# Optimization experiments

Measured on AMD Instinct MI355X. Metric: run time of the kernel, lower is better.

Reference implementation:

```python
import jax, jax.numpy as jnp
import numpy as np

H = 25   # num heads
D = 128  # head dim
EPS = 1e-6

def rmsnorm(x, w):
    # RMSNorm over last dim (hidden=3200), computed in fp32
    var = jnp.mean(jnp.square(x.astype(jnp.float32)), axis=-1, keepdims=True)
    return (x.astype(jnp.float32) * jax.lax.rsqrt(var + EPS)).astype(x.dtype) * w


def setup_inputs() -> dict:
    key = jax.random.key(0)
    ks = jax.random.split(key, 4)
    B, N, C = 8, 1025, 3200
    x = jax.random.normal(ks[0], (B, N, C), dtype=jnp.float32)
    w_qkv = jax.random.normal(ks[1], (3 * C, C), dtype=jnp.float32) * (C ** -0.5)
    q_norm_w = jnp.ones((C,), dtype=jnp.float32)
    k_norm_w = jnp.ones((C,), dtype=jnp.float32)
    w_proj = jax.random.normal(ks[2], (C, C), dtype=jnp.float32) * (C ** -0.5)
    b_proj = jnp.zeros((C,), dtype=jnp.float32)
    return {"x": x, "w_qkv": w_qkv, "q_norm_w": q_norm_w,
            "k_norm_w": k_norm_w, "w_proj": w_proj, "b_proj": b_proj}


def reference(x, w_qkv, q_norm_w, k_norm_w, w_proj, b_proj):
    B, N, C = x.shape
    # fused QKV projection: [B,N,3C]
    qkv = jnp.einsum('bnc,oc->bno', x, w_qkv)
    q, k, v = qkv[..., :C], qkv[..., C:2 * C], qkv[..., 2 * C:]
    # per-tensor RMSNorm over the full hidden dim (flattened across heads)
    q = rmsnorm(q, q_norm_w)
    k = rmsnorm(k, k_norm_w)
    # split heads: [B,N,H,D]
    q = q.reshape(B, N, H, D)
    k = k.reshape(B, N, H, D)
    v = v.reshape(B, N, H, D)
    scale = 1.0 / np.sqrt(D)
    scores = jnp.einsum('bqhd,bkhd->bhqk', q, k) * scale
    attn = jax.nn.softmax(scores, axis=-1)
    out = jnp.einsum('bhqk,bkhd->bqhd', attn, v).reshape(B, N, C)
    return jnp.einsum('bnc,oc->bno', out, w_proj) + b_proj
```

## Files before the change

kernel.cpp:

```cpp
#include <hip/hip_runtime.h>
#include <hip/hip_bf16.h>

#define B_     8
#define N_     1025
#define C_     3200
#define H_     25
#define D_     128
#define NQKV   (3 * C_)
#define NQKVP  9728
#define M_REAL (B_ * N_)
#define M_PAD  8448
#define KVB    64
#define KPAD   1088
#define CPADW  3328

typedef __bf16 bf16x8 __attribute__((ext_vector_type(8)));
typedef short  short8 __attribute__((ext_vector_type(8)));
typedef float  f32x4  __attribute__((ext_vector_type(4)));
typedef unsigned int u32x4 __attribute__((ext_vector_type(4)));

__device__ __forceinline__ unsigned short f2bf(float f) {
    unsigned u = __builtin_bit_cast(unsigned, f);
    u += 0x7FFFu + ((u >> 16) & 1u);
    return (unsigned short)(u >> 16);
}
__device__ __forceinline__ float bf2f(unsigned short u) {
    unsigned v = ((unsigned)u) << 16;
    return __builtin_bit_cast(float, v);
}
__device__ __forceinline__ unsigned cvtpk_bf16(float lo, float hi) {
    unsigned r;
    asm("v_cvt_pk_bf16_f32 %0, %1, %2" : "=v"(r) : "v"(lo), "v"(hi));
    return r;
}
__device__ __forceinline__ void gload_lds16(const unsigned short* g, void* lds) {
    __builtin_amdgcn_global_load_lds(
        (const __attribute__((address_space(1))) void*)g,
        (__attribute__((address_space(3))) void*)lds, 16, 0, 0);
}

__global__ __launch_bounds__(256) void convert_pad(const float* __restrict__ src,
                                                   unsigned short* __restrict__ dst,
                                                   long n_src, long n_tot) {
    long e = ((long)blockIdx.x * 256 + threadIdx.x) * 4;
    if (e >= n_tot) return;
    ushort4 o;
    if (e < n_src) {
        float4 v = *reinterpret_cast<const float4*>(src + e);
        o.x = f2bf(v.x); o.y = f2bf(v.y); o.z = f2bf(v.z); o.w = f2bf(v.w);
    } else {
        o.x = o.y = o.z = o.w = 0;
    }
    *reinterpret_cast<ushort4*>(dst + e) = o;
}

__global__ __launch_bounds__(256) void rmsnorm_qk(unsigned short* __restrict__ qkv,
                                                  const float* __restrict__ qw,
                                                  const float* __restrict__ kw) {
    const int row = blockIdx.x;
    const int seg = blockIdx.y;
    unsigned short* p = qkv + (long)row * NQKVP + seg * C_;
    const float* w = seg ? kw : qw;
    const int t = threadIdx.x;
    const bool has2 = t < (400 - 256);

    short8 v0 = reinterpret_cast<const short8*>(p)[t];
    short8 v1;
    if (has2) v1 = reinterpret_cast<const short8*>(p)[t + 256];

    float s = 0.f;
#pragma unroll
    for (int j = 0; j < 8; ++j) { float f = bf2f((unsigned short)v0[j]); s += f * f; }
    if (has2) {
#pragma unroll
        for (int j = 0; j < 8; ++j) { float f = bf2f((unsigned short)v1[j]); s += f * f; }
    }
#pragma unroll
    for (int m = 32; m; m >>= 1) s += __shfl_xor(s, m);
    __shared__ float red[4];
    if ((t & 63) == 0) red[t >> 6] = s;
    __syncthreads();
    float tot = red[0] + red[1] + red[2] + red[3];
    float scale = rsqrtf(tot * (1.f / C_) + 1e-6f);
    if (seg == 0) scale *= 0.08838834764831845f;

#pragma unroll
    for (int j = 0; j < 8; ++j) {
        float f = bf2f((unsigned short)v0[j]) * scale * w[t * 8 + j];
        v0[j] = (short)f2bf(f);
    }
    reinterpret_cast<short8*>(p)[t] = v0;
    if (has2) {
#pragma unroll
        for (int j = 0; j < 8; ++j) {
            float f = bf2f((unsigned short)v1[j]) * scale * w[(t + 256) * 8 + j];
            v1[j] = (short)f2bf(f);
        }
        reinterpret_cast<short8*>(p)[t + 256] = v1;
    }
}

#define BKT 32
template <int FP32OUT>
__global__ __launch_bounds__(512) void gemm_pipe(const unsigned short* __restrict__ A,
                                                 const unsigned short* __restrict__ Bm,
                                                 unsigned short* __restrict__ Cb,
                                                 float* __restrict__ Cf,
                                                 const float* __restrict__ bias,
                                                 int K, int MT, int NT, int ldc,
                                                 int MStore, int NStore) {
    __shared__ unsigned short sA[4][256 * BKT];
    __shared__ unsigned short sB[4][256 * BKT];

    int bid = blockIdx.x;
    int xcd = bid & 7, pos = bid >> 3;
    int nstrips = NT >> 3;
    int fullpos = nstrips * MT;
    int mt, nt;
    if (pos < fullpos) {
        int strip = pos / MT;
        mt = pos - strip * MT;
        nt = strip * 8 + xcd;
    } else {
        int lin = bid - fullpos * 8;
        nt = nstrips * 8 + lin / MT;
        mt = lin - (lin / MT) * MT;
    }
    const int m0 = mt * 256, n0 = nt * 256;

    const int t = threadIdx.x, w = t >> 6, l = t & 63;
    const int lq = l & 15, lh = l >> 4;
    const int wr = w >> 2, wc = w & 3;

    const unsigned short* Ab = A + (long)m0 * K;
    const unsigned short* Bb = Bm + (long)n0 * K;
    const int nk = K / BKT;

    const int c0 = t, c1 = t + 512;
    const int r0 = c0 >> 2, s0 = (c0 & 3) ^ ((r0 >> 1) & 3);
    const int r1 = c1 >> 2, s1 = (c1 & 3) ^ ((r1 >> 1) & 3);

    f32x4 acc[8][4] = {};

    auto stage = [&](int tile) {
        int k0 = tile * BKT;
        unsigned short* dA = sA[tile & 3];
        unsigned short* dB = sB[tile & 3];
        gload_lds16(Ab + (long)r0 * K + k0 + s0 * 8, (char*)dA + c0 * 16);
        gload_lds16(Ab + (long)r1 * K + k0 + s1 * 8, (char*)dA + c1 * 16);
        gload_lds16(Bb + (long)r0 * K + k0 + s0 * 8, (char*)dB + c0 * 16);
        gload_lds16(Bb + (long)r1 * K + k0 + s1 * 8, (char*)dB + c1 * 16);
    };

    stage(0); stage(1); stage(2);

    for (int tt = 0; tt < nk; ++tt) {
        if (tt + 2 < nk)      asm volatile("s_waitcnt vmcnt(8) lgkmcnt(0)" ::: "memory");
        else if (tt + 1 < nk) asm volatile("s_waitcnt vmcnt(4) lgkmcnt(0)" ::: "memory");
        else                  asm volatile("s_waitcnt vmcnt(0) lgkmcnt(0)" ::: "memory");
        __builtin_amdgcn_s_barrier();

        const unsigned short* bufA = sA[tt & 3];
        const unsigned short* bufB = sB[tt & 3];
        bf16x8 av[8], bv[4];
#pragma unroll
        for (int i = 0; i < 8; ++i) {
            int row = wr * 128 + i * 16 + lq;
            av[i] = *reinterpret_cast<const bf16x8*>(bufA + row * BKT + ((lh ^ ((row >> 1) & 3)) << 3));
        }
#pragma unroll
        for (int j = 0; j < 4; ++j) {
            int row = wc * 64 + j * 16 + lq;
            bv[j] = *reinterpret_cast<const bf16x8*>(bufB + row * BKT + ((lh ^ ((row >> 1) & 3)) << 3));
        }
        if (tt + 3 < nk) stage(tt + 3);

        __builtin_amdgcn_s_setprio(1);
#pragma unroll
        for (int i = 0; i < 8; ++i)
#pragma unroll
            for (int j = 0; j < 4; ++j)
                acc[i][j] = __builtin_amdgcn_mfma_f32_16x16x32_bf16(av[i], bv[j], acc[i][j], 0, 0, 0);
        __builtin_amdgcn_s_setprio(0);
    }

#pragma unroll
    for (int i = 0; i < 8; ++i) {
#pragma unroll
        for (int r2 = 0; r2 < 4; ++r2) {
            long grow = m0 + wr * 128 + i * 16 + lh * 4 + r2;
            if (FP32OUT && grow >= MStore) continue;
#pragma unroll
            for (int j = 0; j < 4; ++j) {
                int gcol = n0 + wc * 64 + j * 16 + lq;
                if (FP32OUT) {
                    if (gcol < NStore)
                        Cf[grow * ldc + gcol] = acc[i][j][r2] + bias[gcol];
                } else {
                    Cb[grow * ldc + gcol] = f2bf(acc[i][j][r2]);
                }
            }
        }
    }
}

__global__ __launch_bounds__(256) void v_transpose(const unsigned short* __restrict__ qkv,
                                                   unsigned short* __restrict__ vtb) {
    const int kt = blockIdx.x, h = blockIdx.y, b = blockIdx.z;
    const int t = threadIdx.x;
    __shared__ unsigned short tile[64][136];

    {
        int r = t >> 2, dq = (t & 3) * 32;
        int key = kt * 64 + r;
        int keyc = key < N_ ? key : N_ - 1;
        const unsigned short* src = qkv + ((long)(b * N_) + keyc) * NQKVP + 2 * C_ + h * D_ + dq;
        short8 a0 = *reinterpret_cast<const short8*>(src);
        short8 a1 = *reinterpret_cast<const short8*>(src + 8);
        short8 a2 = *reinterpret_cast<const short8*>(src + 16);
        short8 a3 = *reinterpret_cast<const short8*>(src + 24);
        if (key >= N_) { a0 = 0; a1 = 0; a2 = 0; a3 = 0; }
        *reinterpret_cast<short8*>(&tile[r][dq])      = a0;
        *reinterpret_cast<short8*>(&tile[r][dq + 8])  = a1;
        *reinterpret_cast<short8*>(&tile[r][dq + 16]) = a2;
        *reinterpret_cast<short8*>(&tile[r][dq + 24]) = a3;
    }
    __syncthreads();
    {
        int d = t >> 1, k0 = (t & 1) * 32;
        unsigned short* dst = vtb + ((long)(b * H_ + h) * D_ + d) * KPAD + kt * 64 + k0;
#pragma unroll
        for (int jj = 0; jj < 4; ++jj) {
            short8 g;
#pragma unroll
            for (int e = 0; e < 8; ++e) g[e] = (short)tile[k0 + jj * 8 + e][d];
            *reinterpret_cast<short8*>(dst + jj * 8) = g;
        }
    }
}

__global__ __launch_bounds__(256, 2) void attn_fwd(const unsigned short* __restrict__ qkv,
                                                   const unsigned short* __restrict__ vtb,
                                                   unsigned short* __restrict__ outb) {
    const int qt = blockIdx.x, h = blockIdx.y, b = blockIdx.z;
    const int t = threadIdx.x, w = t >> 6, l = t & 63;
    const int lq = l & 15, lh = l >> 4;

    __shared__ unsigned short sK[2][KVB * D_];
    __shared__ unsigned short sV[2][D_ * KVB];

    const int qbase = qt * 128 + w * 32;
    bf16x8 qf[2][4];
#pragma unroll
    for (int qg = 0; qg < 2; ++qg) {
        int qrow = qbase + qg * 16 + lq; if (qrow > N_ - 1) qrow = N_ - 1;
        const unsigned short* qp = qkv + (long)(b * N_ + qrow) * NQKVP + h * D_;
#pragma unroll
        for (int ds = 0; ds < 4; ++ds)
            qf[qg][ds] = *reinterpret_cast<const bf16x8*>(qp + ds * 32 + lh * 8);
    }

    const unsigned short* kp[4];
    const unsigned short* vp[4];
#pragma unroll
    for (int i = 0; i < 4; ++i) {
        int slot = i * 256 + t;
        { int r = slot >> 4, sd = (slot & 15) ^ (r & 7);
          kp[i] = qkv + ((long)(b * N_) + r) * NQKVP + C_ + h * D_ + sd * 8; }
        { int d = slot >> 3, sk = (slot & 7) ^ (d & 7);
          vp[i] = vtb + ((long)(b * H_ + h) * D_ + d) * KPAD + sk * 8; }
    }
    const long kvstep = 64L * NQKVP;

    auto stageK = [&](int tile, int buf) {
        char* dst = (char*)sK[buf];
        if (tile < 16) {
            long off = (long)tile * kvstep;
#pragma unroll
            for (int i = 0; i < 4; ++i) gload_lds16(kp[i] + off, dst + (i * 256 + t) * 16);
        } else {
#pragma unroll
            for (int i = 0; i < 4; ++i) {
                int slot = i * 256 + t;
                int r = slot >> 4, sd = (slot & 15) ^ (r & 7);
                const unsigned short* p = qkv + ((long)(b * N_) + (N_ - 1)) * NQKVP + C_ + h * D_ + sd * 8;
                gload_lds16(p, dst + slot * 16);
            }
        }
    };
    auto stageV = [&](int tile, int buf) {
        char* dst = (char*)sV[buf];
        long off = (long)tile * 64;
#pragma unroll
        for (int i = 0; i < 4; ++i) gload_lds16(vp[i] + off, dst + (i * 256 + t) * 16);
    };

    f32x4 o[2][8] = {};
    float m[2] = {-1e30f, -1e30f}, lsum[2] = {0.f, 0.f};

    stageK(0, 0); stageV(0, 0);

    for (int tt = 0; tt < 17; ++tt) {
        const int cur = tt & 1;
        if (tt < 16) { stageK(tt + 1, cur ^ 1); stageV(tt + 1, cur ^ 1); }
        if (tt < 16) asm volatile("s_waitcnt vmcnt(8)" ::: "memory");
        else         asm volatile("s_waitcnt vmcnt(0)" ::: "memory");
        __builtin_amdgcn_s_barrier();

        const unsigned short* bK = sK[cur];
        const unsigned short* bV = sV[cur];

        f32x4 s[2][4] = {};
#pragma unroll
        for (int c = 0; c < 4; ++c) {
            bf16x8 kf[4];
#pragma unroll
            for (int ds = 0; ds < 4; ++ds)
                kf[ds] = *reinterpret_cast<const bf16x8*>(
                    bK + (c * 16 + lq) * D_ + (((ds << 2) + lh) ^ (lq & 7)) * 8);
            __builtin_amdgcn_s_setprio(1);
#pragma unroll
            for (int qg = 0; qg < 2; ++qg)
#pragma unroll
                for (int ds = 0; ds < 4; ++ds)
                    s[qg][c] = __builtin_amdgcn_mfma_f32_16x16x32_bf16(kf[ds], qf[qg][ds], s[qg][c], 0, 0, 0);
            __builtin_amdgcn_s_setprio(0);
        }
        if (tt == 16) {
#pragma unroll
            for (int c = 0; c < 4; ++c)
#pragma unroll
                for (int r = 0; r < 4; ++r)
                    if (c * 16 + 4 * lh + r != 0) { s[0][c][r] = -1e30f; s[1][c][r] = -1e30f; }
        }

        bf16x8 pa[2][2];
#pragma unroll
        for (int qg = 0; qg < 2; ++qg) {
            float mx = s[qg][0][0];
#pragma unroll
            for (int c = 0; c < 4; ++c)
#pragma unroll
                for (int r = 0; r < 4; ++r) mx = fmaxf(mx, s[qg][c][r]);
            mx = fmaxf(mx, __shfl_xor(mx, 16));
            mx = fmaxf(mx, __shfl_xor(mx, 32));
            if (__any(mx - m[qg] > 8.0f)) {
                float mnew = fmaxf(m[qg], mx);
                float corr = __expf(m[qg] - mnew);
                lsum[qg] *= corr;
#pragma unroll
                for (int r = 0; r < 4; ++r) {
                    float co = __shfl(corr, lh * 4 + r);
#pragma unroll
                    for (int nf = 0; nf < 8; ++nf) o[qg][nf][r] *= co;
                }
                m[qg] = mnew;
            }
            float p[4][4]; float rs = 0.f;
#pragma unroll
            for (int c = 0; c < 4; ++c)
#pragma unroll
                for (int r = 0; r < 4; ++r) {
                    p[c][r] = __expf(s[qg][c][r] - m[qg]);
                    rs += p[c][r];
                }
            rs += __shfl_xor(rs, 16);
            rs += __shfl_xor(rs, 32);
            lsum[qg] += rs;
#pragma unroll
            for (int h2 = 0; h2 < 2; ++h2) {
                unsigned A0 = cvtpk_bf16(p[2 * h2][0], p[2 * h2][1]);
                unsigned A1 = cvtpk_bf16(p[2 * h2][2], p[2 * h2][3]);
                unsigned B0 = cvtpk_bf16(p[2 * h2 + 1][0], p[2 * h2 + 1][1]);
                unsigned B1 = cvtpk_bf16(p[2 * h2 + 1][2], p[2 * h2 + 1][3]);
                const bool lo2 = lh < 2, odd = lh & 1;
                unsigned x16_0 = __shfl_xor(lo2 ? A0 : B0, 16);
                unsigned x16_1 = __shfl_xor(lo2 ? A1 : B1, 16);
                unsigned x32_0 = __shfl_xor(lo2 ? B0 : A0, 32);
                unsigned x32_1 = __shfl_xor(lo2 ? B1 : A1, 32);
                unsigned x48_0 = __shfl_xor(odd ? B0 : A0, 48);
                unsigned x48_1 = __shfl_xor(odd ? B1 : A1, 48);
                unsigned w0 = lh == 0 ? A0 : lh == 1 ? x48_0 : lh == 2 ? x32_0 : x16_0;
                unsigned w1 = lh == 0 ? A1 : lh == 1 ? x48_1 : lh == 2 ? x32_1 : x16_1;
                unsigned w2 = lh == 0 ? x16_0 : lh == 1 ? x32_0 : lh == 2 ? x48_0 : B0;
                unsigned w3 = lh == 0 ? x16_1 : lh == 1 ? x32_1 : lh == 2 ? x48_1 : B1;
                u32x4 wv = {w0, w1, w2, w3};
                pa[qg][h2] = __builtin_bit_cast(bf16x8, wv);
            }
        }

#pragma unroll
        for (int h2 = 0; h2 < 2; ++h2) {
            bf16x8 vf[8];
#pragma unroll
            for (int nf = 0; nf < 8; ++nf)
                vf[nf] = *reinterpret_cast<const bf16x8*>(
                    bV + (nf * 16 + lq) * KVB + (((h2 << 2) + lh) ^ (lq & 7)) * 8);
            __builtin_amdgcn_s_setprio(1);
#pragma unroll
            for (int qg = 0; qg < 2; ++qg)
#pragma unroll
                for (int nf = 0; nf < 8; ++nf)
                    o[qg][nf] = __builtin_amdgcn_mfma_f32_16x16x32_bf16(pa[qg][h2], vf[nf], o[qg][nf], 0, 0, 0);
            __builtin_amdgcn_s_setprio(0);
        }
        __builtin_amdgcn_s_barrier();
    }

#pragma unroll
    for (int qg = 0; qg < 2; ++qg) {
        float linv = 1.f / lsum[qg];
#pragma unroll
        for (int r = 0; r < 4; ++r) {
            float li = __shfl(linv, lh * 4 + r);
            int row = qbase + qg * 16 + 4 * lh + r;
            if (row < N_) {
                unsigned short* dst = outb + (long)(b * N_ + row) * C_ + h * D_ + lq;
#pragma unroll
                for (int nf = 0; nf < 8; ++nf)
                    dst[nf * 16] = f2bf(o[qg][nf][r] * li);
            }
        }
    }
}

extern "C" void kernel_launch(void* const* d_in, const int* in_sizes, int n_in,
                              void* d_out, int out_size, void* d_ws, size_t ws_size,
                              hipStream_t stream) {
    (void)in_sizes; (void)n_in; (void)out_size; (void)ws_size;
    const float* x   = (const float*)d_in[0];
    const float* wq  = (const float*)d_in[1];
    const float* qnw = (const float*)d_in[2];
    const float* knw = (const float*)d_in[3];
    const float* wp  = (const float*)d_in[4];
    const float* bp  = (const float*)d_in[5];
    float* out = (float*)d_out;

    unsigned short* xb    = (unsigned short*)d_ws;
    unsigned short* wqb   = xb   + (size_t)M_PAD * C_;
    unsigned short* wpb   = wqb  + (size_t)NQKVP * C_;
    unsigned short* qkvb  = wpb  + (size_t)CPADW * C_;
    unsigned short* attnb = qkvb + (size_t)M_PAD * NQKVP;
    unsigned short* vtb   = wqb;

    auto cvt = [&](const float* s, unsigned short* d, long nsrc, long ntot) {
        int blocks = (int)((ntot / 4 + 255) / 256);
        convert_pad<<<blocks, 256, 0, stream>>>(s, d, nsrc, ntot);
    };
    cvt(x,  xb,  (long)M_REAL * C_, (long)M_PAD * C_);
    cvt(wq, wqb, (long)NQKV * C_,   (long)NQKVP * C_);
    cvt(wp, wpb, (long)C_ * C_,     (long)CPADW * C_);
    cvt(x, attnb + (size_t)M_REAL * C_, 0, (long)(M_PAD - M_REAL) * C_);

    gemm_pipe<0><<<(M_PAD / 256) * (NQKVP / 256), 512, 0, stream>>>(
        xb, wqb, qkvb, nullptr, nullptr, C_, M_PAD / 256, NQKVP / 256, NQKVP, M_PAD, NQKVP);

    rmsnorm_qk<<<dim3(M_REAL, 2), 256, 0, stream>>>(qkvb, qnw, knw);

    v_transpose<<<dim3(17, H_, B_), 256, 0, stream>>>(qkvb, vtb);

    attn_fwd<<<dim3(9, H_, B_), 256, 0, stream>>>(qkvb, vtb, attnb);

    gemm_pipe<1><<<(M_PAD / 256) * (CPADW / 256), 512, 0, stream>>>(
        attnb, wpb, nullptr, out, bp, C_, M_PAD / 256, CPADW / 256, C_, M_REAL, C_);
}
```

Baseline: 1.056 ms.

## Restructure GEMM main loop to BK=64 double buffer with four-phase compute interleaving

Moves the bf16 GEMM from a 4-stage BK=32 LDS ring to a 2-stage BK=64 double buffer, using 8-way XOR swizzled tiles. Each K iteration is split into four quadrant phases, each with its own LDS fragment reads, barriers and MFMA bursts, similar to a ping-pong schedule. The aim is fewer LDS fragment registers, fewer loop iterations per K, and overlap of LDS reads with MFMA work. The cost is a shallower global prefetch depth and many more barriers per iteration, which can expose memory latency.

```diff
diff --git a/kernel.cpp b/kernel.cpp
--- a/kernel.cpp
+++ b/kernel.cpp
@@ -100,7 +100,7 @@
     }
 }
 
-#define BKT 32
+#define BKT 64
 template <int FP32OUT>
 __global__ __launch_bounds__(512) void gemm_pipe(const unsigned short* __restrict__ A,
                                                  const unsigned short* __restrict__ Bm,
@@ -109,8 +109,8 @@
                                                  const float* __restrict__ bias,
                                                  int K, int MT, int NT, int ldc,
                                                  int MStore, int NStore) {
-    __shared__ unsigned short sA[4][256 * BKT];
-    __shared__ unsigned short sB[4][256 * BKT];
+    __shared__ unsigned short sA[2][256 * BKT];
+    __shared__ unsigned short sB[2][256 * BKT];
 
     int bid = blockIdx.x;
     int xcd = bid & 7, pos = bid >> 3;
@@ -136,53 +136,110 @@
     const unsigned short* Bb = Bm + (long)n0 * K;
     const int nk = K / BKT;
 
-    const int c0 = t, c1 = t + 512;
-    const int r0 = c0 >> 2, s0 = (c0 & 3) ^ ((r0 >> 1) & 3);
-    const int r1 = c1 >> 2, s1 = (c1 & 3) ^ ((r1 >> 1) & 3);
-
     f32x4 acc[8][4] = {};
 
     auto stage = [&](int tile) {
         int k0 = tile * BKT;
-        unsigned short* dA = sA[tile & 3];
-        unsigned short* dB = sB[tile & 3];
-        gload_lds16(Ab + (long)r0 * K + k0 + s0 * 8, (char*)dA + c0 * 16);
-        gload_lds16(Ab + (long)r1 * K + k0 + s1 * 8, (char*)dA + c1 * 16);
-        gload_lds16(Bb + (long)r0 * K + k0 + s0 * 8, (char*)dB + c0 * 16);
-        gload_lds16(Bb + (long)r1 * K + k0 + s1 * 8, (char*)dB + c1 * 16);
+        unsigned short* dA = sA[tile & 1];
+        unsigned short* dB = sB[tile & 1];
+#pragma unroll
+        for (int i = 0; i < 4; ++i) {
+            int c = i * 512 + t;
+            int row = c >> 3, sl = (c & 7) ^ (row & 7);
+            gload_lds16(Ab + (long)row * K + k0 + sl * 8, (char*)dA + c * 16);
+            gload_lds16(Bb + (long)row * K + k0 + sl * 8, (char*)dB + c * 16);
+        }
     };
 
-    stage(0); stage(1); stage(2);
+#define RD(buf, row, kk) \
+    (*reinterpret_cast<const bf16x8*>((buf) + (row) * BKT + (((((kk) << 2) + lh)) ^ ((row) & 7)) * 8))
+
+    stage(0);
+    asm volatile("s_waitcnt vmcnt(0)" ::: "memory");
+    __builtin_amdgcn_s_barrier();
 
     for (int tt = 0; tt < nk; ++tt) {
-        if (tt + 2 < nk)      asm volatile("s_waitcnt vmcnt(8) lgkmcnt(0)" ::: "memory");
-        else if (tt + 1 < nk) asm volatile("s_waitcnt vmcnt(4) lgkmcnt(0)" ::: "memory");
-        else                  asm volatile("s_waitcnt vmcnt(0) lgkmcnt(0)" ::: "memory");
-        __builtin_amdgcn_s_barrier();
-
-        const unsigned short* bufA = sA[tt & 3];
-        const unsigned short* bufB = sB[tt & 3];
-        bf16x8 av[8], bv[4];
-#pragma unroll
-        for (int i = 0; i < 8; ++i) {
+        const unsigned short* bufA = sA[tt & 1];
+        const unsigned short* bufB = sB[tt & 1];
+        bf16x8 av[4][2], bv[4][2];
+
+#pragma unroll
+        for (int i = 0; i < 4; ++i) {
             int row = wr * 128 + i * 16 + lq;
-            av[i] = *reinterpret_cast<const bf16x8*>(bufA + row * BKT + ((lh ^ ((row >> 1) & 3)) << 3));
-        }
-#pragma unroll
-        for (int j = 0; j < 4; ++j) {
+            av[i][0] = RD(bufA, row, 0); av[i][1] = RD(bufA, row, 1);
+        }
+#pragma unroll
+        for (int j = 0; j < 2; ++j) {
             int row = wc * 64 + j * 16 + lq;
-            bv[j] = *reinterpret_cast<const bf16x8*>(bufB + row * BKT + ((lh ^ ((row >> 1) & 3)) << 3));
-        }
-        if (tt + 3 < nk) stage(tt + 3);
-
+            bv[j][0] = RD(bufB, row, 0); bv[j][1] = RD(bufB, row, 1);
+        }
+        if (tt + 1 < nk) stage(tt + 1);
+        __builtin_amdgcn_s_barrier();
+        asm volatile("s_waitcnt lgkmcnt(0)" ::: "memory");
+        __builtin_amdgcn_sched_barrier(0);
         __builtin_amdgcn_s_setprio(1);
 #pragma unroll
-        for (int i = 0; i < 8; ++i)
-#pragma unroll
-            for (int j = 0; j < 4; ++j)
-                acc[i][j] = __builtin_amdgcn_mfma_f32_16x16x32_bf16(av[i], bv[j], acc[i][j], 0, 0, 0);
+        for (int i = 0; i < 4; ++i)
+#pragma unroll
+            for (int j = 0; j < 2; ++j) {
+                acc[i][j] = __builtin_amdgcn_mfma_f32_16x16x32_bf16(av[i][0], bv[j][0], acc[i][j], 0, 0, 0);
+                acc[i][j] = __builtin_amdgcn_mfma_f32_16x16x32_bf16(av[i][1], bv[j][1], acc[i][j], 0, 0, 0);
+            }
         __builtin_amdgcn_s_setprio(0);
-    }
+        __builtin_amdgcn_s_barrier();
+
+#pragma unroll
+        for (int j = 2; j < 4; ++j) {
+            int row = wc * 64 + j * 16 + lq;
+            bv[j][0] = RD(bufB, row, 0); bv[j][1] = RD(bufB, row, 1);
+        }
+        __builtin_amdgcn_s_barrier();
+        asm volatile("s_waitcnt lgkmcnt(0)" ::: "memory");
+        __builtin_amdgcn_sched_barrier(0);
+        __builtin_amdgcn_s_setprio(1);
+#pragma unroll
+        for (int i = 0; i < 4; ++i)
+#pragma unroll
+            for (int j = 2; j < 4; ++j) {
+                acc[i][j] = __builtin_amdgcn_mfma_f32_16x16x32_bf16(av[i][0], bv[j][0], acc[i][j], 0, 0, 0);
+                acc[i][j] = __builtin_amdgcn_mfma_f32_16x16x32_bf16(av[i][1], bv[j][1], acc[i][j], 0, 0, 0);
+            }
+        __builtin_amdgcn_s_setprio(0);
+        __builtin_amdgcn_s_barrier();
+
+#pragma unroll
+        for (int i = 0; i < 4; ++i) {
+            int row = wr * 128 + (i + 4) * 16 + lq;
+            av[i][0] = RD(bufA, row, 0); av[i][1] = RD(bufA, row, 1);
+        }
+        __builtin_amdgcn_s_barrier();
+        asm volatile("s_waitcnt lgkmcnt(0)" ::: "memory");
+        __builtin_amdgcn_sched_barrier(0);
+        __builtin_amdgcn_s_setprio(1);
+#pragma unroll
+        for (int i = 0; i < 4; ++i)
+#pragma unroll
+            for (int j = 2; j < 4; ++j) {
+                acc[i + 4][j] = __builtin_amdgcn_mfma_f32_16x16x32_bf16(av[i][0], bv[j][0], acc[i + 4][j], 0, 0, 0);
+                acc[i + 4][j] = __builtin_amdgcn_mfma_f32_16x16x32_bf16(av[i][1], bv[j][1], acc[i + 4][j], 0, 0, 0);
+            }
+        __builtin_amdgcn_s_setprio(0);
+        __builtin_amdgcn_s_barrier();
+
+        asm volatile("s_waitcnt vmcnt(0)" ::: "memory");
+        __builtin_amdgcn_s_barrier();
+        __builtin_amdgcn_s_setprio(1);
+#pragma unroll
+        for (int i = 0; i < 4; ++i)
+#pragma unroll
+            for (int j = 0; j < 2; ++j) {
+                acc[i + 4][j] = __builtin_amdgcn_mfma_f32_16x16x32_bf16(av[i][0], bv[j][0], acc[i + 4][j], 0, 0, 0);
+                acc[i + 4][j] = __builtin_amdgcn_mfma_f32_16x16x32_bf16(av[i][1], bv[j][1], acc[i + 4][j], 0, 0, 0);
+            }
+        __builtin_amdgcn_s_setprio(0);
+        __builtin_amdgcn_s_barrier();
+    }
+#undef RD
 
 #pragma unroll
     for (int i = 0; i < 8; ++i) {
```

New measurement: 1.199 ms. 13.5% more time.
